# Kernel optimization log

Measured on AMD Instinct MI355X. Metric: run time of the kernel, lower is better.

Reference implementation:

```python
import jax, jax.numpy as jnp
import numpy as np

N = 50000      # nodes
E = 800000     # edges (before self-loops)
DIN = 384
D = 128        # hidden_dim == output_dim
H = 4          # heads
FH = D // H    # per-head dim
B = 64         # graphs in batch
NEG = 0.2      # LeakyReLU slope in GATConv
EPS = 1e-5     # LayerNorm eps


def setup_inputs() -> dict:
    key = jax.random.key(0)
    ks = jax.random.split(key, 24)
    s = 0.02
    inp = {
        'node_features': jax.random.normal(ks[0], (N, DIN), jnp.float32),
        'edge_index': jax.random.randint(ks[1], (2, E), 0, N, dtype=jnp.int64),
        'edge_weight': jax.random.uniform(ks[2], (E,), jnp.float32),
        'batch': jnp.sort(jax.random.randint(ks[3], (N,), 0, B, dtype=jnp.int64)),
        # input projection
        'Wp': jax.random.normal(ks[4], (DIN, D), jnp.float32) * s,
        'bp': jnp.zeros((D,), jnp.float32),
    }
    for l in range(2):
        o = 5 + l * 9
        inp[f'W{l}'] = jax.random.normal(ks[o], (D, D), jnp.float32) * s      # lin_src (shared src/dst)
        inp[f'as{l}'] = jax.random.normal(ks[o + 1], (H, FH), jnp.float32) * s  # att_src
        inp[f'ad{l}'] = jax.random.normal(ks[o + 2], (H, FH), jnp.float32) * s  # att_dst
        inp[f'We{l}'] = jax.random.normal(ks[o + 3], (D,), jnp.float32) * s   # lin_edge (edge_dim=1)
        inp[f'ae{l}'] = jax.random.normal(ks[o + 4], (H, FH), jnp.float32) * s  # att_edge
        inp[f'b{l}'] = jnp.zeros((D,), jnp.float32)                           # GATConv bias
        inp[f'g{l}'] = jnp.ones((D,), jnp.float32)                            # LayerNorm gamma
        inp[f'be{l}'] = jnp.zeros((D,), jnp.float32)                          # LayerNorm beta
    return inp


def _gat(x, src, dst, ew, W, a_s, a_d, We, a_e, b):
    """PyG GATConv(in, D/H, heads=H, edge_dim=1), eval mode. ew includes self-loops."""
    n = x.shape[0]
    h = (x @ W).reshape(n, H, FH)                      # [N,H,FH]
    a_src = jnp.einsum('nhf,hf->nh', h, a_s)           # [N,H]
    a_dst = jnp.einsum('nhf,hf->nh', h, a_d)
    e = (ew[:, None] * We[None, :]).reshape(-1, H, FH)  # edge_dim=1 linear, no bias
    a_eg = jnp.einsum('ehf,hf->eh', e, a_e)            # [E,H]
    alpha = jax.nn.leaky_relu(a_src[src] + a_dst[dst] + a_eg, NEG)
    # softmax over incoming edges of each dst node
    amax = jax.ops.segment_max(alpha, dst, num_segments=n)
    amax = jnp.where(jnp.isfinite(amax), amax, 0.0)
    ex = jnp.exp(alpha - amax[dst])
    denom = jax.ops.segment_sum(ex, dst, num_segments=n)
    coef = ex / (denom[dst] + 1e-16)                   # [E,H]
    msg = h[src] * coef[..., None]                     # [E,H,FH]
    out = jax.ops.segment_sum(msg, dst, num_segments=n).reshape(n, D)
    return out + b


def _ln(x, g, b):
    mu = x.mean(-1, keepdims=True)
    v = ((x - mu) ** 2).mean(-1, keepdims=True)
    return (x - mu) * jax.lax.rsqrt(v + EPS) * g + b


def reference(node_features, edge_index, edge_weight, batch, Wp, bp,
              W0, as0, ad0, We0, ae0, b0, g0, be0,
              W1, as1, ad1, We1, ae1, b1, g1, be1):
    n = node_features.shape[0]
    # PyG GATConv add_self_loops=True, fill_value='mean' for edge_attr
    loop = jnp.arange(n, dtype=edge_index.dtype)
    src = jnp.concatenate([edge_index[0], loop])
    dst = jnp.concatenate([edge_index[1], loop])
    ew = jnp.concatenate([edge_weight, jnp.full((n,), edge_weight.mean(), edge_weight.dtype)])

    x = node_features @ Wp + bp
    for (W, a_s, a_d, We, a_e, b, g, be) in (
        (W0, as0, ad0, We0, ae0, b0, g0, be0),
        (W1, as1, ad1, We1, ae1, b1, g1, be1),
    ):
        res = x
        y = _gat(x, src, dst, ew, W, a_s, a_d, We, a_e, b)
        y = jax.nn.elu(_ln(y, g, be))
        x = y + res  # shapes match (hidden == output)

    # global_mean_pool
    s = jax.ops.segment_sum(x, batch, num_segments=B)
    c = jax.ops.segment_sum(jnp.ones((n,), x.dtype), batch, num_segments=B)
    return s / jnp.maximum(c, 1.0)[:, None]
```

## Files before the change

### kernel.cpp

```cpp
#include <hip/hip_runtime.h>

#define N_NODES 50000
#define N_EDGES 800000
#define DIN 384
#define DH 128
#define NB 64
#define NEG 0.2f

__device__ __forceinline__ float bf2f(unsigned short u) {
    return __uint_as_float((unsigned)u << 16);
}
__device__ __forceinline__ unsigned short f2bf(float x) {
    unsigned u = __float_as_uint(x);
    return (unsigned short)((u + 0x7fff + ((u >> 16) & 1)) >> 16);
}
using us8 = __attribute__((ext_vector_type(8))) unsigned short;

__global__ __launch_bounds__(256) void histew_kernel(const int* __restrict__ dst,
                                                     const float* __restrict__ ew,
                                                     int* __restrict__ cnt,
                                                     int* __restrict__ rank,
                                                     float* __restrict__ ews) {
    __shared__ float sred[4];
    const int tid = threadIdx.x;
    float v = 0.0f;
    for (int i = blockIdx.x * 256 + tid; i < N_EDGES; i += gridDim.x * 256) {
        rank[i] = atomicAdd(&cnt[dst[i]], 1);
        v += ew[i];
    }
    #pragma unroll
    for (int o = 32; o; o >>= 1) v += __shfl_down(v, o, 64);
    if ((tid & 63) == 0) sred[tid >> 6] = v;
    __syncthreads();
    if (tid == 0) atomicAdd(ews, sred[0] + sred[1] + sred[2] + sred[3]);
}

__global__ void scan_a(const int* __restrict__ cnt, int* __restrict__ scanned,
                       int* __restrict__ bsums) {
    __shared__ int s[256];
    int tid = threadIdx.x;
    int i = blockIdx.x * 256 + tid;
    int v = (i < N_NODES) ? cnt[i] : 0;
    s[tid] = v; __syncthreads();
    for (int o = 1; o < 256; o <<= 1) {
        int t = (tid >= o) ? s[tid - o] : 0;
        __syncthreads();
        s[tid] += t;
        __syncthreads();
    }
    if (i < N_NODES) scanned[i] = s[tid] - v;
    if (tid == 255) bsums[blockIdx.x] = s[255];
}

__global__ void scan_b(int* __restrict__ bsums, int nb) {
    __shared__ int s[256];
    int tid = threadIdx.x;
    int v = (tid < nb) ? bsums[tid] : 0;
    s[tid] = v; __syncthreads();
    for (int o = 1; o < 256; o <<= 1) {
        int t = (tid >= o) ? s[tid - o] : 0;
        __syncthreads();
        s[tid] += t;
        __syncthreads();
    }
    if (tid < nb) bsums[tid] = s[tid] - v;
}

__global__ void scan_c(const int* __restrict__ scanned, const int* __restrict__ bsums,
                       const int* __restrict__ cnt, int* __restrict__ ptr) {
    int i = blockIdx.x * 256 + threadIdx.x;
    if (i < N_NODES) {
        int p = scanned[i] + bsums[blockIdx.x];
        ptr[i] = p;
        if (i == N_NODES - 1) ptr[N_NODES] = p + cnt[i];
    }
}

__global__ __launch_bounds__(256) void fill_kernel(const int* __restrict__ src,
                            const int* __restrict__ dst,
                            const float* __restrict__ ew,
                            const int* __restrict__ rank,
                            const int* __restrict__ ptr,
                            int4* __restrict__ recQ) {
    const int e0 = (blockIdx.x * 256 + threadIdx.x) * 4;
    if (e0 >= N_EDGES) return;
    const int4 d4 = *(const int4*)(dst + e0);
    const int4 s4 = *(const int4*)(src + e0);
    const int4 r4 = *(const int4*)(rank + e0);
    const float4 w4 = *(const float4*)(ew + e0);
    const int p0 = ptr[d4.x] + r4.x;
    const int p1 = ptr[d4.y] + r4.y;
    const int p2 = ptr[d4.z] + r4.z;
    const int p3 = ptr[d4.w] + r4.w;
    int4 q0 = {s4.x, d4.x, __float_as_int(w4.x), 0};
    int4 q1 = {s4.y, d4.y, __float_as_int(w4.y), 0};
    int4 q2 = {s4.z, d4.z, __float_as_int(w4.z), 0};
    int4 q3 = {s4.w, d4.w, __float_as_int(w4.w), 0};
    recQ[p0] = q0; recQ[p1] = q1; recQ[p2] = q2; recQ[p3] = q3;
}

template<int K, bool BF16OUT>
__global__ __launch_bounds__(256) void mfma_gemm(const float* __restrict__ A,
                                                 const float* __restrict__ W,
                                                 const float* __restrict__ bias,
                                                 void* __restrict__ Cv, int M,
                                                 const float* __restrict__ a_s,
                                                 const float* __restrict__ a_d,
                                                 float* __restrict__ asrc_o,
                                                 float* __restrict__ adst_o)
{
    constexpr int BM = 64, BK = 32;
    constexpr int LS = 40;
    __shared__ unsigned short As[BM * LS];
    __shared__ unsigned short Bs[DH * LS];
    using short8 = __attribute__((ext_vector_type(8))) short;
    using f32x4  = __attribute__((ext_vector_type(4))) float;

    const int tid = threadIdx.x;
    const int w = tid >> 6, l = tid & 63;
    const int lane16 = l & 15, quad = l >> 4;
    const int m0 = blockIdx.x * BM;

    f32x4 acc[8] = {};

    const int ar = tid >> 2, af = tid & 3;
    int arow = m0 + ar; if (arow >= M) arow = M - 1;
    const float* Ap = A + (size_t)arow * K;
    const int bn = tid & 127, bq = tid >> 7;

    for (int k0 = 0; k0 < K; k0 += BK) {
        __syncthreads();
        #pragma unroll
        for (int i = 0; i < 2; ++i) {
            const int f4 = af + 4 * i;
            float4 v = *(const float4*)(Ap + k0 + f4 * 4);
            ushort4 u = {f2bf(v.x), f2bf(v.y), f2bf(v.z), f2bf(v.w)};
            *(ushort4*)&As[ar * LS + f4 * 4] = u;
        }
        #pragma unroll
        for (int i = 0; i < 4; ++i) {
            const int kq = bq + 2 * i;
            float v0 = W[(size_t)(k0 + kq * 4 + 0) * DH + bn];
            float v1 = W[(size_t)(k0 + kq * 4 + 1) * DH + bn];
            float v2 = W[(size_t)(k0 + kq * 4 + 2) * DH + bn];
            float v3 = W[(size_t)(k0 + kq * 4 + 3) * DH + bn];
            ushort4 u = {f2bf(v0), f2bf(v1), f2bf(v2), f2bf(v3)};
            *(ushort4*)&Bs[bn * LS + kq * 4] = u;
        }
        __syncthreads();
        short8 afrag = *(short8*)&As[(w * 16 + lane16) * LS + quad * 8];
        #pragma unroll
        for (int nt = 0; nt < 8; ++nt) {
            short8 bfrag = *(short8*)&Bs[(nt * 16 + lane16) * LS + quad * 8];
            acc[nt] = __builtin_amdgcn_mfma_f32_16x16x32_bf16(afrag, bfrag, acc[nt], 0, 0, 0);
        }
    }

    const int orow0 = m0 + w * 16 + quad * 4;
    #pragma unroll
    for (int nt = 0; nt < 8; ++nt) {
        const int col = nt * 16 + lane16;
        const float bv = BF16OUT ? 0.0f : bias[col];
        #pragma unroll
        for (int r = 0; r < 4; ++r) {
            const int row = orow0 + r;
            if (row < M) {
                if constexpr (BF16OUT)
                    ((unsigned short*)Cv)[(size_t)row * DH + col] = f2bf(acc[nt][r]);
                else
                    ((float*)Cv)[(size_t)row * DH + col] = acc[nt][r] + bv;
            }
        }
    }

    if constexpr (BF16OUT) {
        float psh[4][4] = {}, pdh[4][4] = {};
        #pragma unroll
        for (int nt = 0; nt < 8; ++nt) {
            const int hd = nt >> 1;
            const float asv = a_s[nt * 16 + lane16];
            const float adv = a_d[nt * 16 + lane16];
            #pragma unroll
            for (int r = 0; r < 4; ++r) {
                psh[hd][r] = fmaf(acc[nt][r], asv, psh[hd][r]);
                pdh[hd][r] = fmaf(acc[nt][r], adv, pdh[hd][r]);
            }
        }
        #pragma unroll
        for (int o = 1; o < 16; o <<= 1) {
            #pragma unroll
            for (int hd = 0; hd < 4; ++hd)
                #pragma unroll
                for (int r = 0; r < 4; ++r) {
                    psh[hd][r] += __shfl_xor(psh[hd][r], o, 64);
                    pdh[hd][r] += __shfl_xor(pdh[hd][r], o, 64);
                }
        }
        if (lane16 == 0) {
            #pragma unroll
            for (int r = 0; r < 4; ++r) {
                const int row = orow0 + r;
                if (row < M) {
                    float4 o1 = {psh[0][r], psh[1][r], psh[2][r], psh[3][r]};
                    float4 o2 = {pdh[0][r], pdh[1][r], pdh[2][r], pdh[3][r]};
                    *(float4*)(asrc_o + (size_t)row * 4) = o1;
                    *(float4*)(adst_o + (size_t)row * 4) = o2;
                }
            }
        }
    }
}

__global__ __launch_bounds__(256) void alpha_kernel(
    const int4* __restrict__ recQ, const float* __restrict__ asrc,
    const float* __restrict__ adst, const float* __restrict__ Wedge,
    const float* __restrict__ aedge, float* __restrict__ alQ,
    int* __restrict__ srcQ)
{
    const int l = threadIdx.x & 63;
    float p0 = Wedge[l] * aedge[l];
    float p1 = Wedge[l + 64] * aedge[l + 64];
    #pragma unroll
    for (int o = 1; o < 32; o <<= 1) { p0 += __shfl_xor(p0, o, 64); p1 += __shfl_xor(p1, o, 64); }
    const float cc0 = __shfl(p0, 0, 64), cc1 = __shfl(p0, 32, 64);
    const float cc2 = __shfl(p1, 0, 64), cc3 = __shfl(p1, 32, 64);

    const int e = blockIdx.x * 256 + threadIdx.x;
    if (e >= N_EDGES) return;
    const int4 r = recQ[e];
    const int s = r.x, d = r.y;
    const float wgt = __int_as_float(r.z);
    srcQ[e] = s;
    const float4 a4 = *(const float4*)(asrc + (size_t)s * 4);
    const float4 b4 = *(const float4*)(adst + (size_t)d * 4);
    float v0 = a4.x + b4.x + wgt * cc0;
    float v1 = a4.y + b4.y + wgt * cc1;
    float v2 = a4.z + b4.z + wgt * cc2;
    float v3 = a4.w + b4.w + wgt * cc3;
    v0 = v0 > 0.f ? v0 : NEG * v0;
    v1 = v1 > 0.f ? v1 : NEG * v1;
    v2 = v2 > 0.f ? v2 : NEG * v2;
    v3 = v3 > 0.f ? v3 : NEG * v3;
    float4 o4 = {__expf(v0), __expf(v1), __expf(v2), __expf(v3)};
    *(float4*)(alQ + (size_t)e * 4) = o4;
}

#define MSG_NPB 4
__global__ __launch_bounds__(256) void msg_kernel(
    const unsigned short* __restrict__ h, const float* __restrict__ asrc,
    const float* __restrict__ adst, const float* __restrict__ xres,
    const int* __restrict__ indptr, const int* __restrict__ srcQ,
    const float* __restrict__ alQ, const float* __restrict__ ewsum,
    const float* __restrict__ Wedge, const float* __restrict__ aedge,
    const float* __restrict__ bias, const float* __restrict__ gamma,
    const float* __restrict__ beta, float* __restrict__ xout)
{
    const int l = threadIdx.x & 63;
    const int n = blockIdx.x * MSG_NPB + (threadIdx.x >> 6);
    if (n >= N_NODES) return;
    const int sub2 = l >> 4, c8 = l & 15, hd8 = c8 >> 2;

    float p0 = Wedge[l] * aedge[l];
    float p1 = Wedge[l + 64] * aedge[l + 64];
    #pragma unroll
    for (int o = 1; o < 32; o <<= 1) { p0 += __shfl_xor(p0, o, 64); p1 += __shfl_xor(p1, o, 64); }
    float cc[4];
    cc[0] = __shfl(p0, 0, 64);  cc[1] = __shfl(p0, 32, 64);
    cc[2] = __shfl(p1, 0, 64);  cc[3] = __shfl(p1, 32, 64);

    const float4 ad4 = *(const float4*)(adst + (size_t)n * 4);
    const float4 as4 = *(const float4*)(asrc + (size_t)n * 4);
    const float ewm = ewsum[0] * (1.0f / N_EDGES);
    float pv0[4];
    {
        const float av[4] = {as4.x, as4.y, as4.z, as4.w};
        const float dv[4] = {ad4.x, ad4.y, ad4.z, ad4.w};
        #pragma unroll
        for (int k = 0; k < 4; ++k) {
            float a0 = av[k] + dv[k] + ewm * cc[k];
            a0 = a0 > 0.f ? a0 : NEG * a0;
            pv0[k] = __expf(a0);
        }
    }

    float dsum = 0.f;
    float acc8[8] = {};
    const unsigned short* hb = h + c8 * 8;
    if (sub2 == 0) {
        us8 u = *(const us8*)(hb + (size_t)n * DH);
        const float f = pv0[hd8];
        #pragma unroll
        for (int i = 0; i < 8; ++i) acc8[i] = f * bf2f(u[i]);
    }

    const int st = indptr[n], deg = indptr[n + 1] - st;
    const int* sq = srcQ + st;
    const float* aq = alQ + (size_t)st * 4 + hd8;
    int e = sub2;
    for (; e + 12 < deg; e += 16) {
        const int s0 = sq[e],     s1 = sq[e + 4];
        const int s2 = sq[e + 8], s3 = sq[e + 12];
        const float c0 = aq[(size_t)e * 4],        c1 = aq[(size_t)(e + 4) * 4];
        const float c2 = aq[(size_t)(e + 8) * 4],  c3 = aq[(size_t)(e + 12) * 4];
        us8 u0 = *(const us8*)(hb + (size_t)s0 * DH);
        us8 u1 = *(const us8*)(hb + (size_t)s1 * DH);
        us8 u2 = *(const us8*)(hb + (size_t)s2 * DH);
        us8 u3 = *(const us8*)(hb + (size_t)s3 * DH);
        dsum += c0 + c1 + c2 + c3;
        #pragma unroll
        for (int i = 0; i < 8; ++i)
            acc8[i] = fmaf(c0, bf2f(u0[i]),
                      fmaf(c1, bf2f(u1[i]),
                      fmaf(c2, bf2f(u2[i]),
                      fmaf(c3, bf2f(u3[i]), acc8[i]))));
    }
    for (; e < deg; e += 4) {
        const int s = sq[e];
        const float coef = aq[(size_t)e * 4];
        us8 u = *(const us8*)(hb + (size_t)s * DH);
        dsum += coef;
        #pragma unroll
        for (int i = 0; i < 8; ++i) acc8[i] = fmaf(coef, bf2f(u[i]), acc8[i]);
    }

    #pragma unroll
    for (int i = 0; i < 8; ++i) {
        acc8[i] += __shfl_xor(acc8[i], 16, 64);
        acc8[i] += __shfl_xor(acc8[i], 32, 64);
    }
    dsum += __shfl_xor(dsum, 16, 64);
    dsum += __shfl_xor(dsum, 32, 64);

    const float inv_d = 1.0f / (dsum + pv0[hd8] + 1e-16f);
    const float4 b4a = *(const float4*)(bias + c8 * 8);
    const float4 b4b = *(const float4*)(bias + c8 * 8 + 4);
    float y[8];
    y[0] = acc8[0] * inv_d + b4a.x; y[1] = acc8[1] * inv_d + b4a.y;
    y[2] = acc8[2] * inv_d + b4a.z; y[3] = acc8[3] * inv_d + b4a.w;
    y[4] = acc8[4] * inv_d + b4b.x; y[5] = acc8[5] * inv_d + b4b.y;
    y[6] = acc8[6] * inv_d + b4b.z; y[7] = acc8[7] * inv_d + b4b.w;

    float s1 = 0.f, s2 = 0.f;
    #pragma unroll
    for (int i = 0; i < 8; ++i) { s1 += y[i]; s2 += y[i] * y[i]; }
    #pragma unroll
    for (int o = 1; o < 16; o <<= 1) {
        s1 += __shfl_xor(s1, o, 64);
        s2 += __shfl_xor(s2, o, 64);
    }
    const float mu = s1 * (1.0f / DH);
    const float var = s2 * (1.0f / DH) - mu * mu;
    const float rs = rsqrtf(var + 1e-5f);

    if (sub2 == 0) {
        const float4 g4a = *(const float4*)(gamma + c8 * 8);
        const float4 g4b = *(const float4*)(gamma + c8 * 8 + 4);
        const float4 e4a = *(const float4*)(beta + c8 * 8);
        const float4 e4b = *(const float4*)(beta + c8 * 8 + 4);
        const float4 r4a = *(const float4*)(xres + (size_t)n * DH + c8 * 8);
        const float4 r4b = *(const float4*)(xres + (size_t)n * DH + c8 * 8 + 4);
        const float gv[8] = {g4a.x, g4a.y, g4a.z, g4a.w, g4b.x, g4b.y, g4b.z, g4b.w};
        const float ev[8] = {e4a.x, e4a.y, e4a.z, e4a.w, e4b.x, e4b.y, e4b.z, e4b.w};
        const float rv[8] = {r4a.x, r4a.y, r4a.z, r4a.w, r4b.x, r4b.y, r4b.z, r4b.w};
        float z[8];
        #pragma unroll
        for (int i = 0; i < 8; ++i) {
            float t = (y[i] - mu) * rs * gv[i] + ev[i];
            z[i] = (t > 0.f ? t : __expf(t) - 1.0f) + rv[i];
        }
        *(float4*)(xout + (size_t)n * DH + c8 * 8)     = *(float4*)&z[0];
        *(float4*)(xout + (size_t)n * DH + c8 * 8 + 4) = *(float4*)&z[4];
    }
}

#define PNODES 64
__global__ __launch_bounds__(128) void pool_kernel(const float* __restrict__ x,
        const int* __restrict__ batch, float* __restrict__ pool, int* __restrict__ gcnt)
{
    int t = threadIdx.x;
    int n0 = blockIdx.x * PNODES;
    if (n0 >= N_NODES) return;
    int n1 = min(n0 + PNODES, N_NODES);
    float acc = 0.f; int cn = 0;
    int curb = batch[n0];
    for (int n = n0; n < n1; ++n) {
        int b = batch[n];
        if (b != curb) {
            atomicAdd(&pool[(size_t)curb * DH + t], acc);
            if (t == 0) atomicAdd(&gcnt[curb], cn);
            acc = 0.f; cn = 0; curb = b;
        }
        acc += x[(size_t)n * DH + t];
        ++cn;
    }
    atomicAdd(&pool[(size_t)curb * DH + t], acc);
    if (t == 0) atomicAdd(&gcnt[curb], cn);
}

__global__ void div_kernel(const float* __restrict__ pool, const int* __restrict__ gcnt,
                           float* __restrict__ out)
{
    int i = blockIdx.x * blockDim.x + threadIdx.x;
    if (i < NB * DH) {
        float c = (float)gcnt[i >> 7];
        out[i] = pool[i] / fmaxf(c, 1.0f);
    }
}

extern "C" void kernel_launch(void* const* d_in, const int* in_sizes, int n_in,
                              void* d_out, int out_size, void* d_ws, size_t ws_size,
                              hipStream_t stream)
{
    const float* nf    = (const float*)d_in[0];
    const int*   esrc  = (const int*)d_in[1];
    const int*   edst  = esrc + N_EDGES;
    const float* ew    = (const float*)d_in[2];
    const int*   batch = (const int*)d_in[3];
    const float* Wp    = (const float*)d_in[4];
    const float* bp    = (const float*)d_in[5];
    const float* Wl[2]  = {(const float*)d_in[6],  (const float*)d_in[14]};
    const float* asl[2] = {(const float*)d_in[7],  (const float*)d_in[15]};
    const float* adl[2] = {(const float*)d_in[8],  (const float*)d_in[16]};
    const float* Wel[2] = {(const float*)d_in[9],  (const float*)d_in[17]};
    const float* ael[2] = {(const float*)d_in[10], (const float*)d_in[18]};
    const float* bl[2]  = {(const float*)d_in[11], (const float*)d_in[19]};
    const float* gl[2]  = {(const float*)d_in[12], (const float*)d_in[20]};
    const float* bel[2] = {(const float*)d_in[13], (const float*)d_in[21]};
    float* outp = (float*)d_out;

    char* w = (char*)d_ws;
    auto alloc = [&](size_t bytes) { char* p = w; w += (bytes + 255) & ~255ull; return p; };
    float* xA     = (float*)alloc((size_t)N_NODES * DH * 4);
    float* xB     = (float*)alloc((size_t)N_NODES * DH * 4);
    unsigned short* hbuf = (unsigned short*)alloc((size_t)N_NODES * DH * 2);
    float* asrc   = (float*)alloc((size_t)N_NODES * 4 * 4);
    float* adst   = (float*)alloc((size_t)N_NODES * 4 * 4);
    float* pool   = (float*)alloc((size_t)NB * DH * 4);
    int* gcnt     = (int*)alloc(256);
    float* ews    = (float*)alloc(256);
    int* cnt      = (int*)alloc((size_t)N_NODES * 4);
    int* scanned  = (int*)alloc((size_t)N_NODES * 4);
    int* bsums    = (int*)alloc(1024);
    int* ptr      = (int*)alloc((size_t)(N_NODES + 8) * 4);
    int* rank     = (int*)alloc((size_t)N_EDGES * 4);
    int* srcQ     = (int*)alloc((size_t)N_EDGES * 4);
    int4* recQ    = (int4*)alloc((size_t)N_EDGES * 16);
    float* alQ    = (float*)alloc((size_t)N_EDGES * 4 * 4);

    hipMemsetAsync(pool, 0, (size_t)NB * DH * 4 + 256 + 256 + (size_t)N_NODES * 4, stream);

    const int eb = (N_EDGES + 255) / 256;
    const int sb = (N_NODES + 255) / 256;

    histew_kernel<<<1024, 256, 0, stream>>>(edst, ew, cnt, rank, ews);
    scan_a<<<sb, 256, 0, stream>>>(cnt, scanned, bsums);
    scan_b<<<1, 256, 0, stream>>>(bsums, sb);
    scan_c<<<sb, 256, 0, stream>>>(scanned, bsums, cnt, ptr);
    fill_kernel<<<(N_EDGES / 4 + 255) / 256, 256, 0, stream>>>(esrc, edst, ew, rank, ptr, recQ);

    const int gb = (N_NODES + 63) / 64;
    mfma_gemm<DIN, false><<<gb, 256, 0, stream>>>(nf, Wp, bp, xA, N_NODES,
                                                  nullptr, nullptr, nullptr, nullptr);

    const float* xin = xA;
    float* xout = xB;
    for (int l = 0; l < 2; ++l) {
        mfma_gemm<DH, true><<<gb, 256, 0, stream>>>(xin, Wl[l], nullptr, hbuf, N_NODES,
                                                    asl[l], adl[l], asrc, adst);
        alpha_kernel<<<eb, 256, 0, stream>>>(recQ, asrc, adst, Wel[l], ael[l], alQ, srcQ);
        msg_kernel<<<(N_NODES + MSG_NPB - 1) / MSG_NPB, 256, 0, stream>>>(
            hbuf, asrc, adst, xin, ptr, srcQ, alQ, ews,
            Wel[l], ael[l], bl[l], gl[l], bel[l], xout);
        float* tmp = (float*)xin; xin = xout; xout = tmp;
    }

    pool_kernel<<<(N_NODES + PNODES - 1) / PNODES, 128, 0, stream>>>(xin, batch, pool, gcnt);
    div_kernel<<<(NB * DH + 255) / 256, 256, 0, stream>>>(pool, gcnt, outp);
}
```

Before: 419.9 us.

## Fuse edge attention computation into message kernel and shrink CSR edge records

Removes the separate alpha kernel. The message kernel now gathers asrc per source edge and computes the LeakyReLU/exp attention coefficients inline, so the per-edge alpha and srcQ arrays are no longer written and read back. Edge records shrink from int4 to int2 (src, weight). The edge-attention constants and mean edge weight are precomputed once in scan_b. The message kernel also becomes a grid-stride loop over a fixed 2048-block grid. In exchange, each lane recomputes exp for its head, and there are extra scattered asrc gathers per edge.

```diff
diff --git a/kernel.cpp b/kernel.cpp
--- a/kernel.cpp
+++ b/kernel.cpp
@@ -13,6 +13,13 @@
 __device__ __forceinline__ unsigned short f2bf(float x) {
     unsigned u = __float_as_uint(x);
     return (unsigned short)((u + 0x7fff + ((u >> 16) & 1)) >> 16);
+}
+__device__ __forceinline__ float sel4(float4 v, int k) {
+    float r = v.x;
+    r = (k == 1) ? v.y : r;
+    r = (k == 2) ? v.z : r;
+    r = (k == 3) ? v.w : r;
+    return r;
 }
 using us8 = __attribute__((ext_vector_type(8))) unsigned short;
 
@@ -52,7 +59,10 @@
     if (tid == 255) bsums[blockIdx.x] = s[255];
 }
 
-__global__ void scan_b(int* __restrict__ bsums, int nb) {
+__global__ void scan_b(int* __restrict__ bsums, int nb,
+                       const float* __restrict__ We0, const float* __restrict__ ae0,
+                       const float* __restrict__ We1, const float* __restrict__ ae1,
+                       const float* __restrict__ ews, float* __restrict__ consts) {
     __shared__ int s[256];
     int tid = threadIdx.x;
     int v = (tid < nb) ? bsums[tid] : 0;
@@ -64,6 +74,28 @@
         __syncthreads();
     }
     if (tid < nb) bsums[tid] = s[tid] - v;
+
+    if (tid < 64) {
+        const int l = tid;
+        float p00 = We0[l] * ae0[l];
+        float p01 = We0[l + 64] * ae0[l + 64];
+        float p10 = We1[l] * ae1[l];
+        float p11 = We1[l + 64] * ae1[l + 64];
+        #pragma unroll
+        for (int o = 1; o < 32; o <<= 1) {
+            p00 += __shfl_xor(p00, o, 64); p01 += __shfl_xor(p01, o, 64);
+            p10 += __shfl_xor(p10, o, 64); p11 += __shfl_xor(p11, o, 64);
+        }
+        const float c0 = __shfl(p00, 0, 64), c1 = __shfl(p00, 32, 64);
+        const float c2 = __shfl(p01, 0, 64), c3 = __shfl(p01, 32, 64);
+        const float d0 = __shfl(p10, 0, 64), d1 = __shfl(p10, 32, 64);
+        const float d2 = __shfl(p11, 0, 64), d3 = __shfl(p11, 32, 64);
+        if (l == 0) {
+            consts[0] = c0; consts[1] = c1; consts[2] = c2; consts[3] = c3;
+            consts[4] = d0; consts[5] = d1; consts[6] = d2; consts[7] = d3;
+            consts[8] = ews[0] * (1.0f / N_EDGES);
+        }
+    }
 }
 
 __global__ void scan_c(const int* __restrict__ scanned, const int* __restrict__ bsums,
@@ -81,22 +113,17 @@
                             const float* __restrict__ ew,
                             const int* __restrict__ rank,
                             const int* __restrict__ ptr,
-                            int4* __restrict__ recQ) {
+                            int2* __restrict__ recE) {
     const int e0 = (blockIdx.x * 256 + threadIdx.x) * 4;
     if (e0 >= N_EDGES) return;
     const int4 d4 = *(const int4*)(dst + e0);
     const int4 s4 = *(const int4*)(src + e0);
     const int4 r4 = *(const int4*)(rank + e0);
     const float4 w4 = *(const float4*)(ew + e0);
-    const int p0 = ptr[d4.x] + r4.x;
-    const int p1 = ptr[d4.y] + r4.y;
-    const int p2 = ptr[d4.z] + r4.z;
-    const int p3 = ptr[d4.w] + r4.w;
-    int4 q0 = {s4.x, d4.x, __float_as_int(w4.x), 0};
-    int4 q1 = {s4.y, d4.y, __float_as_int(w4.y), 0};
-    int4 q2 = {s4.z, d4.z, __float_as_int(w4.z), 0};
-    int4 q3 = {s4.w, d4.w, __float_as_int(w4.w), 0};
-    recQ[p0] = q0; recQ[p1] = q1; recQ[p2] = q2; recQ[p3] = q3;
+    recE[ptr[d4.x] + r4.x] = make_int2(s4.x, __float_as_int(w4.x));
+    recE[ptr[d4.y] + r4.y] = make_int2(s4.y, __float_as_int(w4.y));
+    recE[ptr[d4.z] + r4.z] = make_int2(s4.z, __float_as_int(w4.z));
+    recE[ptr[d4.w] + r4.w] = make_int2(s4.w, __float_as_int(w4.w));
 }
 
 template<int K, bool BF16OUT>
@@ -211,165 +238,135 @@
     }
 }
 
-__global__ __launch_bounds__(256) void alpha_kernel(
-    const int4* __restrict__ recQ, const float* __restrict__ asrc,
-    const float* __restrict__ adst, const float* __restrict__ Wedge,
-    const float* __restrict__ aedge, float* __restrict__ alQ,
-    int* __restrict__ srcQ)
-{
-    const int l = threadIdx.x & 63;
-    float p0 = Wedge[l] * aedge[l];
-    float p1 = Wedge[l + 64] * aedge[l + 64];
-    #pragma unroll
-    for (int o = 1; o < 32; o <<= 1) { p0 += __shfl_xor(p0, o, 64); p1 += __shfl_xor(p1, o, 64); }
-    const float cc0 = __shfl(p0, 0, 64), cc1 = __shfl(p0, 32, 64);
-    const float cc2 = __shfl(p1, 0, 64), cc3 = __shfl(p1, 32, 64);
-
-    const int e = blockIdx.x * 256 + threadIdx.x;
-    if (e >= N_EDGES) return;
-    const int4 r = recQ[e];
-    const int s = r.x, d = r.y;
-    const float wgt = __int_as_float(r.z);
-    srcQ[e] = s;
-    const float4 a4 = *(const float4*)(asrc + (size_t)s * 4);
-    const float4 b4 = *(const float4*)(adst + (size_t)d * 4);
-    float v0 = a4.x + b4.x + wgt * cc0;
-    float v1 = a4.y + b4.y + wgt * cc1;
-    float v2 = a4.z + b4.z + wgt * cc2;
-    float v3 = a4.w + b4.w + wgt * cc3;
-    v0 = v0 > 0.f ? v0 : NEG * v0;
-    v1 = v1 > 0.f ? v1 : NEG * v1;
-    v2 = v2 > 0.f ? v2 : NEG * v2;
-    v3 = v3 > 0.f ? v3 : NEG * v3;
-    float4 o4 = {__expf(v0), __expf(v1), __expf(v2), __expf(v3)};
-    *(float4*)(alQ + (size_t)e * 4) = o4;
-}
-
 #define MSG_NPB 4
+#define MSG_GRID 2048
 __global__ __launch_bounds__(256) void msg_kernel(
     const unsigned short* __restrict__ h, const float* __restrict__ asrc,
     const float* __restrict__ adst, const float* __restrict__ xres,
-    const int* __restrict__ indptr, const int* __restrict__ srcQ,
-    const float* __restrict__ alQ, const float* __restrict__ ewsum,
-    const float* __restrict__ Wedge, const float* __restrict__ aedge,
+    const int* __restrict__ indptr, const int2* __restrict__ recE,
+    const float* __restrict__ consts, const int layer,
     const float* __restrict__ bias, const float* __restrict__ gamma,
     const float* __restrict__ beta, float* __restrict__ xout)
 {
     const int l = threadIdx.x & 63;
-    const int n = blockIdx.x * MSG_NPB + (threadIdx.x >> 6);
-    if (n >= N_NODES) return;
+    const int wv = threadIdx.x >> 6;
     const int sub2 = l >> 4, c8 = l & 15, hd8 = c8 >> 2;
 
-    float p0 = Wedge[l] * aedge[l];
-    float p1 = Wedge[l + 64] * aedge[l + 64];
-    #pragma unroll
-    for (int o = 1; o < 32; o <<= 1) { p0 += __shfl_xor(p0, o, 64); p1 += __shfl_xor(p1, o, 64); }
-    float cc[4];
-    cc[0] = __shfl(p0, 0, 64);  cc[1] = __shfl(p0, 32, 64);
-    cc[2] = __shfl(p1, 0, 64);  cc[3] = __shfl(p1, 32, 64);
-
-    const float4 ad4 = *(const float4*)(adst + (size_t)n * 4);
-    const float4 as4 = *(const float4*)(asrc + (size_t)n * 4);
-    const float ewm = ewsum[0] * (1.0f / N_EDGES);
-    float pv0[4];
-    {
-        const float av[4] = {as4.x, as4.y, as4.z, as4.w};
-        const float dv[4] = {ad4.x, ad4.y, ad4.z, ad4.w};
-        #pragma unroll
-        for (int k = 0; k < 4; ++k) {
-            float a0 = av[k] + dv[k] + ewm * cc[k];
-            a0 = a0 > 0.f ? a0 : NEG * a0;
-            pv0[k] = __expf(a0);
-        }
-    }
-
-    float dsum = 0.f;
-    float acc8[8] = {};
+    const float4 ccv = *(const float4*)(consts + layer * 4);
+    const float cc_l = sel4(ccv, hd8);
+    const float ewm = consts[8];
     const unsigned short* hb = h + c8 * 8;
-    if (sub2 == 0) {
-        us8 u = *(const us8*)(hb + (size_t)n * DH);
-        const float f = pv0[hd8];
-        #pragma unroll
-        for (int i = 0; i < 8; ++i) acc8[i] = f * bf2f(u[i]);
-    }
-
-    const int st = indptr[n], deg = indptr[n + 1] - st;
-    const int* sq = srcQ + st;
-    const float* aq = alQ + (size_t)st * 4 + hd8;
-    int e = sub2;
-    for (; e + 12 < deg; e += 16) {
-        const int s0 = sq[e],     s1 = sq[e + 4];
-        const int s2 = sq[e + 8], s3 = sq[e + 12];
-        const float c0 = aq[(size_t)e * 4],        c1 = aq[(size_t)(e + 4) * 4];
-        const float c2 = aq[(size_t)(e + 8) * 4],  c3 = aq[(size_t)(e + 12) * 4];
-        us8 u0 = *(const us8*)(hb + (size_t)s0 * DH);
-        us8 u1 = *(const us8*)(hb + (size_t)s1 * DH);
-        us8 u2 = *(const us8*)(hb + (size_t)s2 * DH);
-        us8 u3 = *(const us8*)(hb + (size_t)s3 * DH);
-        dsum += c0 + c1 + c2 + c3;
-        #pragma unroll
-        for (int i = 0; i < 8; ++i)
-            acc8[i] = fmaf(c0, bf2f(u0[i]),
-                      fmaf(c1, bf2f(u1[i]),
-                      fmaf(c2, bf2f(u2[i]),
-                      fmaf(c3, bf2f(u3[i]), acc8[i]))));
-    }
-    for (; e < deg; e += 4) {
-        const int s = sq[e];
-        const float coef = aq[(size_t)e * 4];
-        us8 u = *(const us8*)(hb + (size_t)s * DH);
-        dsum += coef;
-        #pragma unroll
-        for (int i = 0; i < 8; ++i) acc8[i] = fmaf(coef, bf2f(u[i]), acc8[i]);
-    }
-
-    #pragma unroll
-    for (int i = 0; i < 8; ++i) {
-        acc8[i] += __shfl_xor(acc8[i], 16, 64);
-        acc8[i] += __shfl_xor(acc8[i], 32, 64);
-    }
-    dsum += __shfl_xor(dsum, 16, 64);
-    dsum += __shfl_xor(dsum, 32, 64);
-
-    const float inv_d = 1.0f / (dsum + pv0[hd8] + 1e-16f);
-    const float4 b4a = *(const float4*)(bias + c8 * 8);
-    const float4 b4b = *(const float4*)(bias + c8 * 8 + 4);
-    float y[8];
-    y[0] = acc8[0] * inv_d + b4a.x; y[1] = acc8[1] * inv_d + b4a.y;
-    y[2] = acc8[2] * inv_d + b4a.z; y[3] = acc8[3] * inv_d + b4a.w;
-    y[4] = acc8[4] * inv_d + b4b.x; y[5] = acc8[5] * inv_d + b4b.y;
-    y[6] = acc8[6] * inv_d + b4b.z; y[7] = acc8[7] * inv_d + b4b.w;
-
-    float s1 = 0.f, s2 = 0.f;
-    #pragma unroll
-    for (int i = 0; i < 8; ++i) { s1 += y[i]; s2 += y[i] * y[i]; }
-    #pragma unroll
-    for (int o = 1; o < 16; o <<= 1) {
-        s1 += __shfl_xor(s1, o, 64);
-        s2 += __shfl_xor(s2, o, 64);
-    }
-    const float mu = s1 * (1.0f / DH);
-    const float var = s2 * (1.0f / DH) - mu * mu;
-    const float rs = rsqrtf(var + 1e-5f);
-
-    if (sub2 == 0) {
-        const float4 g4a = *(const float4*)(gamma + c8 * 8);
-        const float4 g4b = *(const float4*)(gamma + c8 * 8 + 4);
-        const float4 e4a = *(const float4*)(beta + c8 * 8);
-        const float4 e4b = *(const float4*)(beta + c8 * 8 + 4);
-        const float4 r4a = *(const float4*)(xres + (size_t)n * DH + c8 * 8);
-        const float4 r4b = *(const float4*)(xres + (size_t)n * DH + c8 * 8 + 4);
-        const float gv[8] = {g4a.x, g4a.y, g4a.z, g4a.w, g4b.x, g4b.y, g4b.z, g4b.w};
-        const float ev[8] = {e4a.x, e4a.y, e4a.z, e4a.w, e4b.x, e4b.y, e4b.z, e4b.w};
-        const float rv[8] = {r4a.x, r4a.y, r4a.z, r4a.w, r4b.x, r4b.y, r4b.z, r4b.w};
-        float z[8];
+
+    for (int n = blockIdx.x * MSG_NPB + wv; n < N_NODES; n += MSG_GRID * MSG_NPB) {
+        const int st = indptr[n];
+        const int deg = indptr[n + 1] - st;
+        const float4 ad4 = *(const float4*)(adst + (size_t)n * 4);
+        const float4 as4 = *(const float4*)(asrc + (size_t)n * 4);
+        const float ad_l = sel4(ad4, hd8);
+        const float as_l = sel4(as4, hd8);
+        float a0 = as_l + ad_l + ewm * cc_l;
+        a0 = a0 > 0.f ? a0 : NEG * a0;
+        const float pv0_l = __expf(a0);
+
+        float dsum = 0.f;
+        float acc8[8] = {};
+        if (sub2 == 0) {
+            us8 u = *(const us8*)(hb + (size_t)n * DH);
+            #pragma unroll
+            for (int i = 0; i < 8; ++i) acc8[i] = pv0_l * bf2f(u[i]);
+        }
+
+        const int2* rq = recE + st;
+        int e = sub2;
+        for (; e + 12 < deg; e += 16) {
+            const int2 r0 = rq[e],     r1 = rq[e + 4];
+            const int2 r2 = rq[e + 8], r3 = rq[e + 12];
+            const float av0 = asrc[(size_t)r0.x * 4 + hd8];
+            const float av1 = asrc[(size_t)r1.x * 4 + hd8];
+            const float av2 = asrc[(size_t)r2.x * 4 + hd8];
+            const float av3 = asrc[(size_t)r3.x * 4 + hd8];
+            us8 u0 = *(const us8*)(hb + (size_t)r0.x * DH);
+            us8 u1 = *(const us8*)(hb + (size_t)r1.x * DH);
+            us8 u2 = *(const us8*)(hb + (size_t)r2.x * DH);
+            us8 u3 = *(const us8*)(hb + (size_t)r3.x * DH);
+            float al0 = av0 + ad_l + __int_as_float(r0.y) * cc_l;
+            float al1 = av1 + ad_l + __int_as_float(r1.y) * cc_l;
+            float al2 = av2 + ad_l + __int_as_float(r2.y) * cc_l;
+            float al3 = av3 + ad_l + __int_as_float(r3.y) * cc_l;
+            al0 = al0 > 0.f ? al0 : NEG * al0;
+            al1 = al1 > 0.f ? al1 : NEG * al1;
+            al2 = al2 > 0.f ? al2 : NEG * al2;
+            al3 = al3 > 0.f ? al3 : NEG * al3;
+            const float c0 = __expf(al0), c1 = __expf(al1);
+            const float c2 = __expf(al2), c3 = __expf(al3);
+            dsum += (c0 + c1) + (c2 + c3);
+            #pragma unroll
+            for (int i = 0; i < 8; ++i)
+                acc8[i] = fmaf(c0, bf2f(u0[i]),
+                          fmaf(c1, bf2f(u1[i]),
+                          fmaf(c2, bf2f(u2[i]),
+                          fmaf(c3, bf2f(u3[i]), acc8[i]))));
+        }
+        for (; e < deg; e += 4) {
+            const int2 r = rq[e];
+            const float av = asrc[(size_t)r.x * 4 + hd8];
+            us8 u = *(const us8*)(hb + (size_t)r.x * DH);
+            float al = av + ad_l + __int_as_float(r.y) * cc_l;
+            al = al > 0.f ? al : NEG * al;
+            const float c = __expf(al);
+            dsum += c;
+            #pragma unroll
+            for (int i = 0; i < 8; ++i) acc8[i] = fmaf(c, bf2f(u[i]), acc8[i]);
+        }
+
         #pragma unroll
         for (int i = 0; i < 8; ++i) {
-            float t = (y[i] - mu) * rs * gv[i] + ev[i];
-            z[i] = (t > 0.f ? t : __expf(t) - 1.0f) + rv[i];
-        }
-        *(float4*)(xout + (size_t)n * DH + c8 * 8)     = *(float4*)&z[0];
-        *(float4*)(xout + (size_t)n * DH + c8 * 8 + 4) = *(float4*)&z[4];
+            acc8[i] += __shfl_xor(acc8[i], 16, 64);
+            acc8[i] += __shfl_xor(acc8[i], 32, 64);
+        }
+        dsum += __shfl_xor(dsum, 16, 64);
+        dsum += __shfl_xor(dsum, 32, 64);
+
+        const float inv_d = 1.0f / (dsum + pv0_l + 1e-16f);
+        const float4 b4a = *(const float4*)(bias + c8 * 8);
+        const float4 b4b = *(const float4*)(bias + c8 * 8 + 4);
+        float y[8];
+        y[0] = acc8[0] * inv_d + b4a.x; y[1] = acc8[1] * inv_d + b4a.y;
+        y[2] = acc8[2] * inv_d + b4a.z; y[3] = acc8[3] * inv_d + b4a.w;
+        y[4] = acc8[4] * inv_d + b4b.x; y[5] = acc8[5] * inv_d + b4b.y;
+        y[6] = acc8[6] * inv_d + b4b.z; y[7] = acc8[7] * inv_d + b4b.w;
+
+        float s1 = 0.f, s2 = 0.f;
+        #pragma unroll
+        for (int i = 0; i < 8; ++i) { s1 += y[i]; s2 += y[i] * y[i]; }
+        #pragma unroll
+        for (int o = 1; o < 16; o <<= 1) {
+            s1 += __shfl_xor(s1, o, 64);
+            s2 += __shfl_xor(s2, o, 64);
+        }
+        const float mu = s1 * (1.0f / DH);
+        const float var = s2 * (1.0f / DH) - mu * mu;
+        const float rs = rsqrtf(var + 1e-5f);
+
+        if (sub2 == 0) {
+            const float4 g4a = *(const float4*)(gamma + c8 * 8);
+            const float4 g4b = *(const float4*)(gamma + c8 * 8 + 4);
+            const float4 e4a = *(const float4*)(beta + c8 * 8);
+            const float4 e4b = *(const float4*)(beta + c8 * 8 + 4);
+            const float4 r4a = *(const float4*)(xres + (size_t)n * DH + c8 * 8);
+            const float4 r4b = *(const float4*)(xres + (size_t)n * DH + c8 * 8 + 4);
+            const float gv[8] = {g4a.x, g4a.y, g4a.z, g4a.w, g4b.x, g4b.y, g4b.z, g4b.w};
+            const float ev[8] = {e4a.x, e4a.y, e4a.z, e4a.w, e4b.x, e4b.y, e4b.z, e4b.w};
+            const float rv[8] = {r4a.x, r4a.y, r4a.z, r4a.w, r4b.x, r4b.y, r4b.z, r4b.w};
+            float z[8];
+            #pragma unroll
+            for (int i = 0; i < 8; ++i) {
+                float t = (y[i] - mu) * rs * gv[i] + ev[i];
+                z[i] = (t > 0.f ? t : __expf(t) - 1.0f) + rv[i];
+            }
+            *(float4*)(xout + (size_t)n * DH + c8 * 8)     = *(float4*)&z[0];
+            *(float4*)(xout + (size_t)n * DH + c8 * 8 + 4) = *(float4*)&z[4];
+        }
     }
 }
 
@@ -443,20 +440,18 @@
     int* bsums    = (int*)alloc(1024);
     int* ptr      = (int*)alloc((size_t)(N_NODES + 8) * 4);
     int* rank     = (int*)alloc((size_t)N_EDGES * 4);
-    int* srcQ     = (int*)alloc((size_t)N_EDGES * 4);
-    int4* recQ    = (int4*)alloc((size_t)N_EDGES * 16);
-    float* alQ    = (float*)alloc((size_t)N_EDGES * 4 * 4);
+    int2* recE    = (int2*)alloc((size_t)N_EDGES * 8);
+    float* consts = (float*)alloc(256);
 
     hipMemsetAsync(pool, 0, (size_t)NB * DH * 4 + 256 + 256 + (size_t)N_NODES * 4, stream);
 
-    const int eb = (N_EDGES + 255) / 256;
     const int sb = (N_NODES + 255) / 256;
 
     histew_kernel<<<1024, 256, 0, stream>>>(edst, ew, cnt, rank, ews);
     scan_a<<<sb, 256, 0, stream>>>(cnt, scanned, bsums);
-    scan_b<<<1, 256, 0, stream>>>(bsums, sb);
+    scan_b<<<1, 256, 0, stream>>>(bsums, sb, Wel[0], ael[0], Wel[1], ael[1], ews, consts);
     scan_c<<<sb, 256, 0, stream>>>(scanned, bsums, cnt, ptr);
-    fill_kernel<<<(N_EDGES / 4 + 255) / 256, 256, 0, stream>>>(esrc, edst, ew, rank, ptr, recQ);
+    fill_kernel<<<(N_EDGES / 4 + 255) / 256, 256, 0, stream>>>(esrc, edst, ew, rank, ptr, recE);
 
     const int gb = (N_NODES + 63) / 64;
     mfma_gemm<DIN, false><<<gb, 256, 0, stream>>>(nf, Wp, bp, xA, N_NODES,
@@ -467,10 +462,9 @@
     for (int l = 0; l < 2; ++l) {
         mfma_gemm<DH, true><<<gb, 256, 0, stream>>>(xin, Wl[l], nullptr, hbuf, N_NODES,
                                                     asl[l], adl[l], asrc, adst);
-        alpha_kernel<<<eb, 256, 0, stream>>>(recQ, asrc, adst, Wel[l], ael[l], alQ, srcQ);
-        msg_kernel<<<(N_NODES + MSG_NPB - 1) / MSG_NPB, 256, 0, stream>>>(
-            hbuf, asrc, adst, xin, ptr, srcQ, alQ, ews,
-            Wel[l], ael[l], bl[l], gl[l], bel[l], xout);
+        msg_kernel<<<MSG_GRID, 256, 0, stream>>>(
+            hbuf, asrc, adst, xin, ptr, recE, consts, l,
+            bl[l], gl[l], bel[l], xout);
         float* tmp = (float*)xin; xin = xout; xout = tmp;
     }
 
```

Result: no change. 418.5 us (-0.3%).
